# Performance work log

Measured on AMD Instinct MI355X. Metric: run time of the kernel, lower is better.

Reference implementation:

```python
import jax, jax.numpy as jnp
import numpy as np

NUM_HEADS = 16
NEG_INF = float('-inf')


def setup_inputs() -> dict:
    key = jax.random.key(0)
    ks = jax.random.split(key, 8)
    B, S, D = 2, 2048, 1024
    return {
        "query": jax.random.normal(ks[0], (B, S, D), jnp.float32),
        "key": jax.random.normal(ks[1], (B, S, D), jnp.float32),
        "value": jax.random.normal(ks[2], (B, S, D), jnp.float32),
        "attention_mask": jnp.zeros((B, S, S), dtype=bool),
        "Wq": jax.random.normal(ks[3], (D, D), jnp.float32) * (D ** -0.5),
        "Wk": jax.random.normal(ks[4], (D, D), jnp.float32) * (D ** -0.5),
        "Wv": jax.random.normal(ks[5], (D, D), jnp.float32) * (D ** -0.5),
        "Wout": jax.random.normal(ks[6], (D, D), jnp.float32) * (D ** -0.5),
        "b_out": jnp.zeros((D,), jnp.float32),
        "is_causal": 1,
    }


def reference(query, key, value, attention_mask, Wq, Wk, Wv, Wout, b_out, is_causal):
    B, q_len, D = query.shape
    k_len = key.shape[1]
    H = NUM_HEADS
    dk = D // H
    # projections (torch Linear: x @ W.T), split heads -> [B, H, S, dk]
    q = (query @ Wq.T).reshape(B, q_len, H, dk).transpose(0, 2, 1, 3)
    k = (key @ Wk.T).reshape(B, k_len, H, dk).transpose(0, 2, 1, 3)
    v = (value @ Wv.T).reshape(B, k_len, H, dk).transpose(0, 2, 1, 3)
    scores = jnp.einsum('bhqd,bhkd->bhqk', q, k) / jnp.sqrt(jnp.float32(dk))
    if is_causal:
        causal = jnp.triu(jnp.ones((q_len, k_len), dtype=bool), k=1)
        scores = jnp.where(causal, NEG_INF, scores)
    # attn_mask True -> masked out; broadcast over heads
    scores = jnp.where(attention_mask[:, None, :, :], NEG_INF, scores)
    attn = jax.nn.softmax(scores, axis=-1)
    attn = jnp.where(jnp.isnan(attn), 0.0, attn)  # fully-masked rows -> 0
    out = jnp.einsum('bhqk,bhkd->bhqd', attn, v)
    out = out.transpose(0, 2, 1, 3).reshape(B, q_len, D)
    return out @ Wout.T + b_out
```

## Files before the change

### kernel.cpp

```cpp
#include <hip/hip_runtime.h>
#include <hip/hip_bf16.h>

typedef __attribute__((ext_vector_type(8))) short bf16x8;
typedef __attribute__((ext_vector_type(4))) float f32x4;
typedef unsigned long long u64;
typedef unsigned int u32;

#define MFMA(a,b,c) __builtin_amdgcn_mfma_f32_16x16x32_bf16(a,b,c,0,0,0)
#define NEG_INF (-__builtin_inff())
#define SCALE2 0.1803368801111244f

__device__ __forceinline__ unsigned short f2b(float f) {
  unsigned int u = __float_as_uint(f);
  u = u + 0x7fffu + ((u >> 16) & 1u);
  return (unsigned short)(u >> 16);
}

__device__ __forceinline__ u32 pkbf(float lo, float hi) {
  __hip_bfloat162 h = __float22bfloat162_rn(float2{lo, hi});
  return *reinterpret_cast<u32*>(&h);
}

__device__ __forceinline__ void gload_lds16(const unsigned short* g, unsigned short* l) {
  __builtin_amdgcn_global_load_lds((const __attribute__((address_space(1))) void*)g,
                                   (__attribute__((address_space(3))) void*)l, 16, 0, 0);
}

__global__ void cvt7(const float* s0, const float* s1, const float* s2,
                     const float* s3, const float* s4, const float* s5, const float* s6,
                     unsigned short* d0, unsigned short* d1, unsigned short* d2,
                     unsigned short* d3, unsigned short* d4, unsigned short* d5, unsigned short* d6,
                     int nbig, int nsmall) {
  const float* s; unsigned short* d; int n4;
  switch (blockIdx.y) {
    case 0: s=s0; d=d0; n4=nbig; break;
    case 1: s=s1; d=d1; n4=nbig; break;
    case 2: s=s2; d=d2; n4=nbig; break;
    case 3: s=s3; d=d3; n4=nsmall; break;
    case 4: s=s4; d=d4; n4=nsmall; break;
    case 5: s=s5; d=d5; n4=nsmall; break;
    default: s=s6; d=d6; n4=nsmall; break;
  }
  int i = blockIdx.x * blockDim.x + threadIdx.x;
  if (i < n4) {
    float4 v = reinterpret_cast<const float4*>(s)[i];
    ushort4 o;
    o.x = f2b(v.x); o.y = f2b(v.y); o.z = f2b(v.z); o.w = f2b(v.w);
    reinterpret_cast<ushort4*>(d)[i] = o;
  }
}

__global__ void pack_mask(const unsigned char* __restrict__ am, u64* __restrict__ pm, int nU) {
  int lane = threadIdx.x & 63;
  int wid = blockIdx.x * (blockDim.x >> 6) + (threadIdx.x >> 6);
  int stride = gridDim.x * (blockDim.x >> 6);
  for (int u = wid; u < nU; u += stride) {
    unsigned char v = am[(size_t)u * 64 + lane];
    u64 m = __ballot(v != 0);
    if (lane == 0) pm[u] = m;
  }
}

__global__ void mask_summary(const u64* __restrict__ pm, u32* __restrict__ ms, int rows, int nkt) {
  int lane = threadIdx.x & 63;
  int wid = (blockIdx.x * blockDim.x + threadIdx.x) >> 6;
  int nw = (gridDim.x * blockDim.x) >> 6;
  for (int rp = wid; rp < (rows >> 1); rp += nw) {
    int row = rp * 2 + (lane >> 5);
    int t = lane & 31;
    u64 v = pm[(size_t)row * nkt + t];
    u64 bm = __ballot(v != 0ULL);
    if (lane == 0)  ms[rp*2]     = (u32)bm;
    if (lane == 32) ms[rp*2 + 1] = (u32)(bm >> 32);
  }
}

__global__ __launch_bounds__(256) void qkv128s(
    const unsigned short* __restrict__ A,
    const unsigned short* __restrict__ Bw,
    unsigned short* __restrict__ Cqk,
    unsigned short* __restrict__ Cv)
{
  const int K = 1024;
  __shared__ unsigned short As[128*32];
  __shared__ unsigned short Bs[128*32];
  const int tid  = threadIdx.x;
  const int w    = tid >> 6, lane = tid & 63;
  const int wr   = w >> 1,   wc   = w & 1;
  const int g    = lane >> 4, li  = lane & 15;
  const int m0   = blockIdx.x * 128, n0 = blockIdx.y * 128;
  const int bq0  = (m0 >> 12) * 1024 + n0;

  f32x4 acc[4][4] = {};

  const int rS0 = (w*2+0)*16 + (lane>>2);
  const int rS1 = (w*2+1)*16 + (lane>>2);
  const int cS  = (lane&3)*8;
  const unsigned short* gA0 = A  + (size_t)(m0+rS0)*K + cS;
  const unsigned short* gA1 = A  + (size_t)(m0+rS1)*K + cS;
  const unsigned short* gB0 = Bw + (size_t)(bq0+rS0)*K + cS;
  const unsigned short* gB1 = Bw + (size_t)(bq0+rS1)*K + cS;
  unsigned short* lA0 = &As[(w*2+0)*512];
  unsigned short* lA1 = &As[(w*2+1)*512];
  unsigned short* lB0 = &Bs[(w*2+0)*512];
  unsigned short* lB1 = &Bs[(w*2+1)*512];

  for (int k0 = 0; k0 < K; k0 += 32) {
    gload_lds16(gA0 + k0, lA0);
    gload_lds16(gA1 + k0, lA1);
    gload_lds16(gB0 + k0, lB0);
    gload_lds16(gB1 + k0, lB1);
    __syncthreads();

    bf16x8 af[4], bf[4];
    #pragma unroll
    for (int i = 0; i < 4; ++i)
      af[i] = *(const bf16x8*)(&As[(wr*64 + i*16 + li)*32 + g*8]);
    #pragma unroll
    for (int j = 0; j < 4; ++j)
      bf[j] = *(const bf16x8*)(&Bs[(wc*64 + j*16 + li)*32 + g*8]);
    #pragma unroll
    for (int i = 0; i < 4; ++i)
      #pragma unroll
      for (int j = 0; j < 4; ++j)
        acc[i][j] = MFMA(af[i], bf[j], acc[i][j]);
    __syncthreads();
  }

  #pragma unroll
  for (int i = 0; i < 4; ++i) {
    #pragma unroll
    for (int j = 0; j < 4; ++j) {
      int col = n0 + wc*64 + j*16 + li;
      #pragma unroll
      for (int r = 0; r < 4; ++r) {
        int row = m0 + wr*64 + i*16 + g*4 + r;
        float v = acc[i][j][r];
        if (row < 8192) {
          size_t addr = (((size_t)(row >> 11) * 16 + (col >> 6)) * 2048 + (row & 2047)) * 64 + (col & 63);
          Cqk[addr] = f2b(v);
        } else {
          int tk = row & 4095;
          size_t addr = (((size_t)(tk >> 11) * 16 + (col >> 6)) * 64 + (col & 63)) * 2048 + (tk & 2047);
          Cv[addr] = f2b(v);
        }
      }
    }
  }
}

__global__ __launch_bounds__(256) void gemm64db(
    const unsigned short* __restrict__ A,
    const unsigned short* __restrict__ Bw,
    float* __restrict__ Cf,
    const float* __restrict__ bias,
    int M, int N, int K)
{
  const int NT = 32;
  __shared__ unsigned short As[2][64*32];
  __shared__ unsigned short Bs[2][128*32];
  const int tid  = threadIdx.x;
  const int w    = tid >> 6, lane = tid & 63;
  const int wr   = w >> 1,   wc   = w & 1;
  const int g    = lane >> 4, li  = lane & 15;
  const int m0   = blockIdx.x * 64, n0 = blockIdx.y * 128;

  f32x4 acc[2][4] = {};
  const int crow = lane >> 2, ccol = (lane & 3) * 8;
  const unsigned short* gA  = A  + (size_t)(m0 + w*16 + crow)*K + ccol;
  const unsigned short* gB0 = Bw + (size_t)(n0 + w*16 + crow)*K + ccol;
  const unsigned short* gB1 = Bw + (size_t)(n0 + (w+4)*16 + crow)*K + ccol;

  gload_lds16(gA,  &As[0][w*512]);
  gload_lds16(gB0, &Bs[0][w*512]);
  gload_lds16(gB1, &Bs[0][(w+4)*512]);
  __syncthreads();

  for (int t = 0; t < NT; ++t) {
    const int cur = t & 1;
    if (t + 1 < NT) {
      const int k1 = (t + 1) * 32;
      gload_lds16(gA  + k1, &As[cur^1][w*512]);
      gload_lds16(gB0 + k1, &Bs[cur^1][w*512]);
      gload_lds16(gB1 + k1, &Bs[cur^1][(w+4)*512]);
    }
    bf16x8 af[2], bf[4];
    #pragma unroll
    for (int i = 0; i < 2; ++i)
      af[i] = *(const bf16x8*)(&As[cur][(wr*32 + i*16 + li)*32 + g*8]);
    #pragma unroll
    for (int j = 0; j < 4; ++j)
      bf[j] = *(const bf16x8*)(&Bs[cur][(wc*64 + j*16 + li)*32 + g*8]);
    #pragma unroll
    for (int i = 0; i < 2; ++i)
      #pragma unroll
      for (int j = 0; j < 4; ++j)
        acc[i][j] = MFMA(af[i], bf[j], acc[i][j]);
    __syncthreads();
  }

  #pragma unroll
  for (int i = 0; i < 2; ++i) {
    #pragma unroll
    for (int j = 0; j < 4; ++j) {
      int col = n0 + wc*64 + j*16 + li;
      #pragma unroll
      for (int r = 0; r < 4; ++r) {
        int row = m0 + wr*32 + i*16 + g*4 + r;
        Cf[(size_t)row*N + col] = acc[i][j][r] + bias[col];
      }
    }
  }
}

__global__ __launch_bounds__(256, 4) void attn_kernel(
    const unsigned short* __restrict__ Qh,
    const unsigned short* __restrict__ Kh,
    const unsigned short* __restrict__ Vt,
    const u64* __restrict__ pmask,
    const u32* __restrict__ msum,
    const int* __restrict__ causal_p,
    unsigned short* __restrict__ Ob,
    int B, int H, int S)
{
  __shared__ unsigned short Ks [64*64];
  __shared__ unsigned short Vts[64*64];

  const int tid = threadIdx.x, w = tid >> 6, lane = tid & 63;
  const int g = lane >> 4, li = lane & 15;
  const int nkt = S >> 6, nqt = S >> 6;
  const int causal = causal_p[0];

  int id = blockIdx.x;
  int par = (id ^ (id >> 8)) & 1;
  int qh  = ((id >> 1) & 15) ^ (((id >> 8) & 3) << 2);
  int bh  = id >> 5;
  int qt  = par ? (nqt - 1 - qh) : qh;
  const int q0 = qt << 6;
  const int b = bh / H, h = bh % H;
  const size_t baseK = (size_t)bh * S * 64;
  const size_t baseV = (size_t)bh * 64 * S;

  const int qg = q0 + w*16 + li;
  const unsigned short* qp = Qh + baseK + (size_t)qg*64 + g*8;
  const bf16x8 qf0 = *(const bf16x8*)(qp);
  const bf16x8 qf1 = *(const bf16x8*)(qp + 32);

  const u32 sOr = msum[(size_t)b*S + qg];

  f32x4 oacc[4] = {};
  float mrun = -1e30f, lrun = 0.f;

  const int colk  = (lane & 7) ^ ((lane >> 3) & 7);
  const int ldrow = lane >> 3;
  const int ntile = causal ? (qt + 1) : nkt;

  for (int t = 0; t < ntile; ++t) {
    const int kv0 = t << 6;
    __syncthreads();
    #pragma unroll
    for (int s2 = 0; s2 < 2; ++s2) {
      int u = w*2 + s2;
      gload_lds16(Kh + baseK + (size_t)(kv0 + u*8 + ldrow)*64 + colk*8, &Ks[u*512]);
      gload_lds16(Vt + baseV + (size_t)(u*8 + ldrow)*S + kv0 + colk*8, &Vts[u*512]);
    }
    __syncthreads();

    f32x4 sa[4];
    #pragma unroll
    for (int ni = 0; ni < 4; ++ni) sa[ni] = (f32x4){0.f, 0.f, 0.f, 0.f};
    #pragma unroll
    for (int ni = 0; ni < 4; ++ni) {
      int row = ni*16 + li, rx = row & 7;
      bf16x8 k0 = *(const bf16x8*)(&Ks[row*64 + ((g     ^ rx))*8]);
      bf16x8 k1 = *(const bf16x8*)(&Ks[row*64 + (((4+g) ^ rx))*8]);
      sa[ni] = MFMA(k0, qf0, sa[ni]);
      sa[ni] = MFMA(k1, qf1, sa[ni]);
    }

    const bool edge   = (causal != 0) && (t == ntile - 1);
    const bool doMask = __any(((sOr >> t) & 1u) != 0u);
    float corr = 1.0f;
    bool rescale = true;

    if (!edge && !doMask) {
      float pe[4][4];
      #pragma unroll
      for (int ni = 0; ni < 4; ++ni)
        #pragma unroll
        for (int r = 0; r < 4; ++r)
          pe[ni][r] = exp2f(fmaf(sa[ni][r], SCALE2, -mrun));
      float a0 = fmaxf(sa[0][0], sa[0][1]), a1 = fmaxf(sa[0][2], sa[0][3]);
      float a2 = fmaxf(sa[1][0], sa[1][1]), a3 = fmaxf(sa[1][2], sa[1][3]);
      float a4 = fmaxf(sa[2][0], sa[2][1]), a5 = fmaxf(sa[2][2], sa[2][3]);
      float a6 = fmaxf(sa[3][0], sa[3][1]), a7 = fmaxf(sa[3][2], sa[3][3]);
      float mx = fmaxf(fmaxf(fmaxf(a0,a1), fmaxf(a2,a3)),
                       fmaxf(fmaxf(a4,a5), fmaxf(a6,a7)));
      mx = fmaxf(mx, __shfl_xor(mx, 16));
      mx = fmaxf(mx, __shfl_xor(mx, 32));
      float mxs = mx * SCALE2;
      if (__all(mxs <= mrun + 8.0f)) {
        float s0 = (pe[0][0]+pe[0][1]) + (pe[0][2]+pe[0][3]);
        float s1 = (pe[1][0]+pe[1][1]) + (pe[1][2]+pe[1][3]);
        float s2 = (pe[2][0]+pe[2][1]) + (pe[2][2]+pe[2][3]);
        float s3 = (pe[3][0]+pe[3][1]) + (pe[3][2]+pe[3][3]);
        float rs = (s0+s1) + (s2+s3);
        rs += __shfl_xor(rs, 16);
        rs += __shfl_xor(rs, 32);
        lrun += rs;
        #pragma unroll
        for (int ni = 0; ni < 4; ++ni)
          #pragma unroll
          for (int r = 0; r < 4; ++r)
            sa[ni][r] = pe[ni][r];
        rescale = false;
      } else {
        float mu = fmaxf(mrun, mxs);
        corr = exp2f(mrun - mu);
        float rs = 0.f;
        #pragma unroll
        for (int ni = 0; ni < 4; ++ni)
          #pragma unroll
          for (int r = 0; r < 4; ++r) {
            float p = exp2f(fmaf(sa[ni][r], SCALE2, -mu));
            sa[ni][r] = p;
            rs += p;
          }
        rs += __shfl_xor(rs, 16);
        rs += __shfl_xor(rs, 32);
        lrun = lrun * corr + rs;
        mrun = mu;
      }
    } else {
      u64 mrow = doMask ? pmask[((size_t)b*S + qg) * nkt + t] : 0ULL;
      #pragma unroll
      for (int ni = 0; ni < 4; ++ni)
        #pragma unroll
        for (int r = 0; r < 4; ++r) {
          int kvloc = ni*16 + g*4 + r;
          bool dead = (edge && (kv0 + kvloc > qg)) || ((mrow >> kvloc) & 1ULL);
          sa[ni][r] = dead ? NEG_INF : sa[ni][r] * SCALE2;
        }
      float mx = sa[0][0];
      #pragma unroll
      for (int ni = 0; ni < 4; ++ni)
        #pragma unroll
        for (int r = 0; r < 4; ++r)
          if (ni + r) mx = fmaxf(mx, sa[ni][r]);
      mx = fmaxf(mx, __shfl_xor(mx, 16));
      mx = fmaxf(mx, __shfl_xor(mx, 32));
      float mu = fmaxf(mrun, mx);
      corr = exp2f(mrun - mu);
      float rs = 0.f;
      #pragma unroll
      for (int ni = 0; ni < 4; ++ni)
        #pragma unroll
        for (int r = 0; r < 4; ++r) {
          float pe = exp2f(sa[ni][r] - mu);
          sa[ni][r] = pe;
          rs += pe;
        }
      rs += __shfl_xor(rs, 16);
      rs += __shfl_xor(rs, 32);
      lrun = lrun * corr + rs;
      mrun = mu;
    }

    bf16x8 pf[2];
    #pragma unroll
    for (int c = 0; c < 2; ++c) {
      u32 PA0 = pkbf(sa[2*c  ][0], sa[2*c  ][1]);
      u32 PA1 = pkbf(sa[2*c  ][2], sa[2*c  ][3]);
      u32 PB0 = pkbf(sa[2*c+1][0], sa[2*c+1][1]);
      u32 PB1 = pkbf(sa[2*c+1][2], sa[2*c+1][3]);
      u32 X16_0 = (u32)__shfl_xor((int)((g==2) ? PB0 : PA0), 16);
      u32 X16_1 = (u32)__shfl_xor((int)((g==2) ? PB1 : PA1), 16);
      u32 X32_0 = (u32)__shfl_xor((int)((g==0) ? PB0 : PA0), 32);
      u32 X32_1 = (u32)__shfl_xor((int)((g==0) ? PB1 : PA1), 32);
      u32 X48_0 = (u32)__shfl_xor((int)((g==1) ? PB0 : PA0), 48);
      u32 X48_1 = (u32)__shfl_xor((int)((g==1) ? PB1 : PA1), 48);
      union { u32 u[4]; bf16x8 v; } pbu;
      pbu.u[0] = (g==0) ? PA0   : (g==1) ? X48_0 : (g==2) ? X32_0 : X16_0;
      pbu.u[1] = (g==0) ? PA1   : (g==1) ? X48_1 : (g==2) ? X32_1 : X16_1;
      pbu.u[2] = (g==0) ? X16_0 : (g==1) ? X32_0 : (g==2) ? X48_0 : PB0;
      pbu.u[3] = (g==0) ? X16_1 : (g==1) ? X32_1 : (g==2) ? X48_1 : PB1;
      pf[c] = pbu.v;
    }

    if (rescale) {
      #pragma unroll
      for (int di = 0; di < 4; ++di) {
        oacc[di][0] *= corr; oacc[di][1] *= corr;
        oacc[di][2] *= corr; oacc[di][3] *= corr;
      }
    }

    #pragma unroll
    for (int c = 0; c < 2; ++c) {
      #pragma unroll
      for (int di = 0; di < 4; ++di) {
        int d = di*16 + li;
        bf16x8 vf = *(const bf16x8*)(&Vts[d*64 + (((c*4+g) ^ (d&7)))*8]);
        oacc[di] = MFMA(vf, pf[c], oacc[di]);
      }
    }
  }

  __syncthreads();
  unsigned short* scr = &Ks[w*1024];
  float rl = (lrun > 0.f) ? 1.0f / lrun : 0.f;
  #pragma unroll
  for (int di = 0; di < 4; ++di)
    #pragma unroll
    for (int r = 0; r < 4; ++r) {
      int d = di*16 + g*4 + r;
      scr[li*64 + (((d>>3) ^ (li&7)))*8 + (d&7)] = f2b(oacc[di][r] * rl);
    }
  const int D = H * 64;
  #pragma unroll
  for (int rr = 0; rr < 2; ++rr) {
    int q = rr*8 + (lane >> 3);
    int sl = lane & 7;
    bf16x8 v = *(const bf16x8*)(&scr[q*64 + ((sl ^ (q & 7)))*8]);
    *(bf16x8*)(Ob + (size_t)(b*S + q0 + w*16 + q)*D + h*64 + sl*8) = v;
  }
}

extern "C" void kernel_launch(void* const* d_in, const int* in_sizes, int n_in,
                              void* d_out, int out_size, void* d_ws, size_t ws_size,
                              hipStream_t stream) {
  const float* query = (const float*)d_in[0];
  const float* key_  = (const float*)d_in[1];
  const float* value = (const float*)d_in[2];
  const unsigned char* amask = (const unsigned char*)d_in[3];
  const float* Wq   = (const float*)d_in[4];
  const float* Wk   = (const float*)d_in[5];
  const float* Wv   = (const float*)d_in[6];
  const float* Wout = (const float*)d_in[7];
  const float* b_out = (const float*)d_in[8];
  const int* is_causal = (const int*)d_in[9];
  float* out = (float*)d_out;

  const int B = 2, S = 2048, D = 1024, H = 16;
  const int M = B * S;
  const size_t nx = (size_t)M * D;
  const size_t nw = (size_t)D * D;
  const int nU = B * S * (S / 64);

  unsigned short* ws = (unsigned short*)d_ws;
  unsigned short* xq = ws;
  unsigned short* xk = xq + nx;
  unsigned short* xv = xk + nx;
  unsigned short* wq = xv + nx;
  unsigned short* wk = wq + nw;
  unsigned short* wv = wk + nw;
  unsigned short* wo = wv + nw;
  unsigned short* qb = wo + nw;
  unsigned short* kb = qb + nx;
  unsigned short* vt = kb + nx;
  u32* msum = (u32*)(vt + nx);
  unsigned short* ob = xq;
  u64* pmask = (u64*)xv;

  cvt7<<<dim3((unsigned)(nx/4/256), 7), 256, 0, stream>>>(
      query, key_, value, Wq, Wk, Wv, Wout,
      xq, xk, xv, wq, wk, wv, wo, (int)(nx/4), (int)(nw/4));

  qkv128s<<<dim3(3*M/128, D/128), 256, 0, stream>>>(xq, wq, qb, vt);

  pack_mask<<<512, 256, 0, stream>>>(amask, pmask, nU);
  mask_summary<<<128, 256, 0, stream>>>(pmask, msum, M, S/64);

  attn_kernel<<<dim3((S/64) * B * H), 256, 0, stream>>>(qb, kb, vt, pmask, msum, is_causal, ob, B, H, S);

  gemm64db<<<dim3(M/64, D/128), 256, 0, stream>>>(ob, wo, out, b_out, M, D, D);
}
```

Baseline: 168.3 us.

## Pair low and high causal query tiles per block to share K/V loads

Each attention block now handles two query tiles, qt and nqt-1-qt, so causal work is balanced across blocks. The K/V tiles loaded into LDS are reused by both query tiles, which roughly halves global K/V traffic for the low tile. The grid shrinks to 512 blocks, each doing more work with double the accumulator registers. This may lower occupancy and cut parallelism on a large GPU. The bh=id&31 indexing hardcodes B*H=32.

```diff
diff --git a/kernel.cpp b/kernel.cpp
--- a/kernel.cpp
+++ b/kernel.cpp
@@ -213,6 +213,151 @@
   }
 }
 
+__device__ __forceinline__ void attn_tile(
+    const unsigned short* __restrict__ Ks, const unsigned short* __restrict__ Vts,
+    const bf16x8& qf0, const bf16x8& qf1,
+    float& mrun, float& lrun, f32x4* oacc,
+    bool edge, bool doMask, const u64* __restrict__ prow,
+    int t, int kv0, int qg, int g, int li)
+{
+  f32x4 sa[4];
+  #pragma unroll
+  for (int ni = 0; ni < 4; ++ni) sa[ni] = (f32x4){0.f, 0.f, 0.f, 0.f};
+  #pragma unroll
+  for (int ni = 0; ni < 4; ++ni) {
+    int row = ni*16 + li, rx = row & 7;
+    bf16x8 k0 = *(const bf16x8*)(&Ks[row*64 + ((g     ^ rx))*8]);
+    bf16x8 k1 = *(const bf16x8*)(&Ks[row*64 + (((4+g) ^ rx))*8]);
+    sa[ni] = MFMA(k0, qf0, sa[ni]);
+    sa[ni] = MFMA(k1, qf1, sa[ni]);
+  }
+
+  float corr = 1.0f;
+  bool rescale = true;
+
+  if (!edge && !doMask) {
+    float pe[4][4];
+    #pragma unroll
+    for (int ni = 0; ni < 4; ++ni)
+      #pragma unroll
+      for (int r = 0; r < 4; ++r)
+        pe[ni][r] = exp2f(fmaf(sa[ni][r], SCALE2, -mrun));
+    float a0 = fmaxf(sa[0][0], sa[0][1]), a1 = fmaxf(sa[0][2], sa[0][3]);
+    float a2 = fmaxf(sa[1][0], sa[1][1]), a3 = fmaxf(sa[1][2], sa[1][3]);
+    float a4 = fmaxf(sa[2][0], sa[2][1]), a5 = fmaxf(sa[2][2], sa[2][3]);
+    float a6 = fmaxf(sa[3][0], sa[3][1]), a7 = fmaxf(sa[3][2], sa[3][3]);
+    float mx = fmaxf(fmaxf(fmaxf(a0,a1), fmaxf(a2,a3)),
+                     fmaxf(fmaxf(a4,a5), fmaxf(a6,a7)));
+    mx = fmaxf(mx, __shfl_xor(mx, 16));
+    mx = fmaxf(mx, __shfl_xor(mx, 32));
+    float mxs = mx * SCALE2;
+    if (__all(mxs <= mrun + 8.0f)) {
+      float s0 = (pe[0][0]+pe[0][1]) + (pe[0][2]+pe[0][3]);
+      float s1 = (pe[1][0]+pe[1][1]) + (pe[1][2]+pe[1][3]);
+      float s2 = (pe[2][0]+pe[2][1]) + (pe[2][2]+pe[2][3]);
+      float s3 = (pe[3][0]+pe[3][1]) + (pe[3][2]+pe[3][3]);
+      float rs = (s0+s1) + (s2+s3);
+      rs += __shfl_xor(rs, 16);
+      rs += __shfl_xor(rs, 32);
+      lrun += rs;
+      #pragma unroll
+      for (int ni = 0; ni < 4; ++ni)
+        #pragma unroll
+        for (int r = 0; r < 4; ++r)
+          sa[ni][r] = pe[ni][r];
+      rescale = false;
+    } else {
+      float mu = fmaxf(mrun, mxs);
+      corr = exp2f(mrun - mu);
+      float rs = 0.f;
+      #pragma unroll
+      for (int ni = 0; ni < 4; ++ni)
+        #pragma unroll
+        for (int r = 0; r < 4; ++r) {
+          float p = exp2f(fmaf(sa[ni][r], SCALE2, -mu));
+          sa[ni][r] = p;
+          rs += p;
+        }
+      rs += __shfl_xor(rs, 16);
+      rs += __shfl_xor(rs, 32);
+      lrun = lrun * corr + rs;
+      mrun = mu;
+    }
+  } else {
+    u64 mrow = doMask ? prow[t] : 0ULL;
+    #pragma unroll
+    for (int ni = 0; ni < 4; ++ni)
+      #pragma unroll
+      for (int r = 0; r < 4; ++r) {
+        int kvloc = ni*16 + g*4 + r;
+        bool dead = (edge && (kv0 + kvloc > qg)) || ((mrow >> kvloc) & 1ULL);
+        sa[ni][r] = dead ? NEG_INF : sa[ni][r] * SCALE2;
+      }
+    float mx = sa[0][0];
+    #pragma unroll
+    for (int ni = 0; ni < 4; ++ni)
+      #pragma unroll
+      for (int r = 0; r < 4; ++r)
+        if (ni + r) mx = fmaxf(mx, sa[ni][r]);
+    mx = fmaxf(mx, __shfl_xor(mx, 16));
+    mx = fmaxf(mx, __shfl_xor(mx, 32));
+    float mu = fmaxf(mrun, mx);
+    corr = exp2f(mrun - mu);
+    float rs = 0.f;
+    #pragma unroll
+    for (int ni = 0; ni < 4; ++ni)
+      #pragma unroll
+      for (int r = 0; r < 4; ++r) {
+        float pe = exp2f(sa[ni][r] - mu);
+        sa[ni][r] = pe;
+        rs += pe;
+      }
+    rs += __shfl_xor(rs, 16);
+    rs += __shfl_xor(rs, 32);
+    lrun = lrun * corr + rs;
+    mrun = mu;
+  }
+
+  bf16x8 pf[2];
+  #pragma unroll
+  for (int c = 0; c < 2; ++c) {
+    u32 PA0 = pkbf(sa[2*c  ][0], sa[2*c  ][1]);
+    u32 PA1 = pkbf(sa[2*c  ][2], sa[2*c  ][3]);
+    u32 PB0 = pkbf(sa[2*c+1][0], sa[2*c+1][1]);
+    u32 PB1 = pkbf(sa[2*c+1][2], sa[2*c+1][3]);
+    u32 X16_0 = (u32)__shfl_xor((int)((g==2) ? PB0 : PA0), 16);
+    u32 X16_1 = (u32)__shfl_xor((int)((g==2) ? PB1 : PA1), 16);
+    u32 X32_0 = (u32)__shfl_xor((int)((g==0) ? PB0 : PA0), 32);
+    u32 X32_1 = (u32)__shfl_xor((int)((g==0) ? PB1 : PA1), 32);
+    u32 X48_0 = (u32)__shfl_xor((int)((g==1) ? PB0 : PA0), 48);
+    u32 X48_1 = (u32)__shfl_xor((int)((g==1) ? PB1 : PA1), 48);
+    union { u32 u[4]; bf16x8 v; } pbu;
+    pbu.u[0] = (g==0) ? PA0   : (g==1) ? X48_0 : (g==2) ? X32_0 : X16_0;
+    pbu.u[1] = (g==0) ? PA1   : (g==1) ? X48_1 : (g==2) ? X32_1 : X16_1;
+    pbu.u[2] = (g==0) ? X16_0 : (g==1) ? X32_0 : (g==2) ? X48_0 : PB0;
+    pbu.u[3] = (g==0) ? X16_1 : (g==1) ? X32_1 : (g==2) ? X48_1 : PB1;
+    pf[c] = pbu.v;
+  }
+
+  if (rescale) {
+    #pragma unroll
+    for (int di = 0; di < 4; ++di) {
+      oacc[di][0] *= corr; oacc[di][1] *= corr;
+      oacc[di][2] *= corr; oacc[di][3] *= corr;
+    }
+  }
+
+  #pragma unroll
+  for (int c = 0; c < 2; ++c) {
+    #pragma unroll
+    for (int di = 0; di < 4; ++di) {
+      int d = di*16 + li;
+      bf16x8 vf = *(const bf16x8*)(&Vts[d*64 + (((c*4+g) ^ (d&7)))*8]);
+      oacc[di] = MFMA(vf, pf[c], oacc[di]);
+    }
+  }
+}
+
 __global__ __launch_bounds__(256, 4) void attn_kernel(
     const unsigned short* __restrict__ Qh,
     const unsigned short* __restrict__ Kh,
@@ -228,34 +373,42 @@
 
   const int tid = threadIdx.x, w = tid >> 6, lane = tid & 63;
   const int g = lane >> 4, li = lane & 15;
-  const int nkt = S >> 6, nqt = S >> 6;
+  const int nkt = S >> 6;
   const int causal = causal_p[0];
 
-  int id = blockIdx.x;
-  int par = (id ^ (id >> 8)) & 1;
-  int qh  = ((id >> 1) & 15) ^ (((id >> 8) & 3) << 2);
-  int bh  = id >> 5;
-  int qt  = par ? (nqt - 1 - qh) : qh;
-  const int q0 = qt << 6;
-  const int b = bh / H, h = bh % H;
+  const int id = blockIdx.x;
+  const int bh = id & 31;
+  const int qp = id >> 5;
+  const int qtL = qp, qtH = nkt - 1 - qp;
+  const int q0L = qtL << 6, q0H = qtH << 6;
+  const int b = bh >> 4, h = bh & 15;
   const size_t baseK = (size_t)bh * S * 64;
   const size_t baseV = (size_t)bh * 64 * S;
 
-  const int qg = q0 + w*16 + li;
-  const unsigned short* qp = Qh + baseK + (size_t)qg*64 + g*8;
-  const bf16x8 qf0 = *(const bf16x8*)(qp);
-  const bf16x8 qf1 = *(const bf16x8*)(qp + 32);
-
-  const u32 sOr = msum[(size_t)b*S + qg];
-
-  f32x4 oacc[4] = {};
-  float mrun = -1e30f, lrun = 0.f;
+  const int qgL = q0L + w*16 + li;
+  const int qgH = q0H + w*16 + li;
+  const unsigned short* qpL = Qh + baseK + (size_t)qgL*64 + g*8;
+  const unsigned short* qpH = Qh + baseK + (size_t)qgH*64 + g*8;
+  const bf16x8 qfL0 = *(const bf16x8*)(qpL);
+  const bf16x8 qfL1 = *(const bf16x8*)(qpL + 32);
+  const bf16x8 qfH0 = *(const bf16x8*)(qpH);
+  const bf16x8 qfH1 = *(const bf16x8*)(qpH + 32);
+
+  const u32 sOrL = msum[(size_t)b*S + qgL];
+  const u32 sOrH = msum[(size_t)b*S + qgH];
+  const u64* prowL = pmask + (size_t)(b*S + qgL) * nkt;
+  const u64* prowH = pmask + (size_t)(b*S + qgH) * nkt;
+
+  f32x4 oaccL[4] = {}, oaccH[4] = {};
+  float mrunL = -1e30f, lrunL = 0.f;
+  float mrunH = -1e30f, lrunH = 0.f;
 
   const int colk  = (lane & 7) ^ ((lane >> 3) & 7);
   const int ldrow = lane >> 3;
-  const int ntile = causal ? (qt + 1) : nkt;
-
-  for (int t = 0; t < ntile; ++t) {
+  const int ntL = causal ? (qtL + 1) : nkt;
+  const int ntH = causal ? (qtH + 1) : nkt;
+
+  for (int t = 0; t < ntH; ++t) {
     const int kv0 = t << 6;
     __syncthreads();
     #pragma unroll
@@ -266,163 +419,43 @@
     }
     __syncthreads();
 
-    f32x4 sa[4];
-    #pragma unroll
-    for (int ni = 0; ni < 4; ++ni) sa[ni] = (f32x4){0.f, 0.f, 0.f, 0.f};
-    #pragma unroll
-    for (int ni = 0; ni < 4; ++ni) {
-      int row = ni*16 + li, rx = row & 7;
-      bf16x8 k0 = *(const bf16x8*)(&Ks[row*64 + ((g     ^ rx))*8]);
-      bf16x8 k1 = *(const bf16x8*)(&Ks[row*64 + (((4+g) ^ rx))*8]);
-      sa[ni] = MFMA(k0, qf0, sa[ni]);
-      sa[ni] = MFMA(k1, qf1, sa[ni]);
-    }
-
-    const bool edge   = (causal != 0) && (t == ntile - 1);
-    const bool doMask = __any(((sOr >> t) & 1u) != 0u);
-    float corr = 1.0f;
-    bool rescale = true;
-
-    if (!edge && !doMask) {
-      float pe[4][4];
-      #pragma unroll
-      for (int ni = 0; ni < 4; ++ni)
-        #pragma unroll
-        for (int r = 0; r < 4; ++r)
-          pe[ni][r] = exp2f(fmaf(sa[ni][r], SCALE2, -mrun));
-      float a0 = fmaxf(sa[0][0], sa[0][1]), a1 = fmaxf(sa[0][2], sa[0][3]);
-      float a2 = fmaxf(sa[1][0], sa[1][1]), a3 = fmaxf(sa[1][2], sa[1][3]);
-      float a4 = fmaxf(sa[2][0], sa[2][1]), a5 = fmaxf(sa[2][2], sa[2][3]);
-      float a6 = fmaxf(sa[3][0], sa[3][1]), a7 = fmaxf(sa[3][2], sa[3][3]);
-      float mx = fmaxf(fmaxf(fmaxf(a0,a1), fmaxf(a2,a3)),
-                       fmaxf(fmaxf(a4,a5), fmaxf(a6,a7)));
-      mx = fmaxf(mx, __shfl_xor(mx, 16));
-      mx = fmaxf(mx, __shfl_xor(mx, 32));
-      float mxs = mx * SCALE2;
-      if (__all(mxs <= mrun + 8.0f)) {
-        float s0 = (pe[0][0]+pe[0][1]) + (pe[0][2]+pe[0][3]);
-        float s1 = (pe[1][0]+pe[1][1]) + (pe[1][2]+pe[1][3]);
-        float s2 = (pe[2][0]+pe[2][1]) + (pe[2][2]+pe[2][3]);
-        float s3 = (pe[3][0]+pe[3][1]) + (pe[3][2]+pe[3][3]);
-        float rs = (s0+s1) + (s2+s3);
-        rs += __shfl_xor(rs, 16);
-        rs += __shfl_xor(rs, 32);
-        lrun += rs;
-        #pragma unroll
-        for (int ni = 0; ni < 4; ++ni)
-          #pragma unroll
-          for (int r = 0; r < 4; ++r)
-            sa[ni][r] = pe[ni][r];
-        rescale = false;
-      } else {
-        float mu = fmaxf(mrun, mxs);
-        corr = exp2f(mrun - mu);
-        float rs = 0.f;
-        #pragma unroll
-        for (int ni = 0; ni < 4; ++ni)
-          #pragma unroll
-          for (int r = 0; r < 4; ++r) {
-            float p = exp2f(fmaf(sa[ni][r], SCALE2, -mu));
-            sa[ni][r] = p;
-            rs += p;
-          }
-        rs += __shfl_xor(rs, 16);
-        rs += __shfl_xor(rs, 32);
-        lrun = lrun * corr + rs;
-        mrun = mu;
-      }
-    } else {
-      u64 mrow = doMask ? pmask[((size_t)b*S + qg) * nkt + t] : 0ULL;
-      #pragma unroll
-      for (int ni = 0; ni < 4; ++ni)
-        #pragma unroll
-        for (int r = 0; r < 4; ++r) {
-          int kvloc = ni*16 + g*4 + r;
-          bool dead = (edge && (kv0 + kvloc > qg)) || ((mrow >> kvloc) & 1ULL);
-          sa[ni][r] = dead ? NEG_INF : sa[ni][r] * SCALE2;
-        }
-      float mx = sa[0][0];
-      #pragma unroll
-      for (int ni = 0; ni < 4; ++ni)
-        #pragma unroll
-        for (int r = 0; r < 4; ++r)
-          if (ni + r) mx = fmaxf(mx, sa[ni][r]);
-      mx = fmaxf(mx, __shfl_xor(mx, 16));
-      mx = fmaxf(mx, __shfl_xor(mx, 32));
-      float mu = fmaxf(mrun, mx);
-      corr = exp2f(mrun - mu);
-      float rs = 0.f;
-      #pragma unroll
-      for (int ni = 0; ni < 4; ++ni)
-        #pragma unroll
-        for (int r = 0; r < 4; ++r) {
-          float pe = exp2f(sa[ni][r] - mu);
-          sa[ni][r] = pe;
-          rs += pe;
-        }
-      rs += __shfl_xor(rs, 16);
-      rs += __shfl_xor(rs, 32);
-      lrun = lrun * corr + rs;
-      mrun = mu;
-    }
-
-    bf16x8 pf[2];
-    #pragma unroll
-    for (int c = 0; c < 2; ++c) {
-      u32 PA0 = pkbf(sa[2*c  ][0], sa[2*c  ][1]);
-      u32 PA1 = pkbf(sa[2*c  ][2], sa[2*c  ][3]);
-      u32 PB0 = pkbf(sa[2*c+1][0], sa[2*c+1][1]);
-      u32 PB1 = pkbf(sa[2*c+1][2], sa[2*c+1][3]);
-      u32 X16_0 = (u32)__shfl_xor((int)((g==2) ? PB0 : PA0), 16);
-      u32 X16_1 = (u32)__shfl_xor((int)((g==2) ? PB1 : PA1), 16);
-      u32 X32_0 = (u32)__shfl_xor((int)((g==0) ? PB0 : PA0), 32);
-      u32 X32_1 = (u32)__shfl_xor((int)((g==0) ? PB1 : PA1), 32);
-      u32 X48_0 = (u32)__shfl_xor((int)((g==1) ? PB0 : PA0), 48);
-      u32 X48_1 = (u32)__shfl_xor((int)((g==1) ? PB1 : PA1), 48);
-      union { u32 u[4]; bf16x8 v; } pbu;
-      pbu.u[0] = (g==0) ? PA0   : (g==1) ? X48_0 : (g==2) ? X32_0 : X16_0;
-      pbu.u[1] = (g==0) ? PA1   : (g==1) ? X48_1 : (g==2) ? X32_1 : X16_1;
-      pbu.u[2] = (g==0) ? X16_0 : (g==1) ? X32_0 : (g==2) ? X48_0 : PB0;
-      pbu.u[3] = (g==0) ? X16_1 : (g==1) ? X32_1 : (g==2) ? X48_1 : PB1;
-      pf[c] = pbu.v;
-    }
-
-    if (rescale) {
-      #pragma unroll
-      for (int di = 0; di < 4; ++di) {
-        oacc[di][0] *= corr; oacc[di][1] *= corr;
-        oacc[di][2] *= corr; oacc[di][3] *= corr;
-      }
-    }
-
-    #pragma unroll
-    for (int c = 0; c < 2; ++c) {
-      #pragma unroll
-      for (int di = 0; di < 4; ++di) {
-        int d = di*16 + li;
-        bf16x8 vf = *(const bf16x8*)(&Vts[d*64 + (((c*4+g) ^ (d&7)))*8]);
-        oacc[di] = MFMA(vf, pf[c], oacc[di]);
-      }
+    {
+      const bool edge   = (causal != 0) && (t == ntH - 1);
+      const bool doMask = __any(((sOrH >> t) & 1u) != 0u);
+      attn_tile(Ks, Vts, qfH0, qfH1, mrunH, lrunH, oaccH,
+                edge, doMask, prowH, t, kv0, qgH, g, li);
+    }
+    if (t < ntL) {
+      const bool edge   = (causal != 0) && (t == ntL - 1);
+      const bool doMask = __any(((sOrL >> t) & 1u) != 0u);
+      attn_tile(Ks, Vts, qfL0, qfL1, mrunL, lrunL, oaccL,
+                edge, doMask, prowL, t, kv0, qgL, g, li);
     }
   }
 
   __syncthreads();
-  unsigned short* scr = &Ks[w*1024];
-  float rl = (lrun > 0.f) ? 1.0f / lrun : 0.f;
+  const int D = H * 64;
+  unsigned short* scrL = &Ks[w*1024];
+  unsigned short* scrH = &Vts[w*1024];
+  float rlL = (lrunL > 0.f) ? 1.0f / lrunL : 0.f;
+  float rlH = (lrunH > 0.f) ? 1.0f / lrunH : 0.f;
   #pragma unroll
   for (int di = 0; di < 4; ++di)
     #pragma unroll
     for (int r = 0; r < 4; ++r) {
       int d = di*16 + g*4 + r;
-      scr[li*64 + (((d>>3) ^ (li&7)))*8 + (d&7)] = f2b(oacc[di][r] * rl);
-    }
-  const int D = H * 64;
+      int slot = ((d>>3) ^ (li&7));
+      scrL[li*64 + slot*8 + (d&7)] = f2b(oaccL[di][r] * rlL);
+      scrH[li*64 + slot*8 + (d&7)] = f2b(oaccH[di][r] * rlH);
+    }
   #pragma unroll
   for (int rr = 0; rr < 2; ++rr) {
     int q = rr*8 + (lane >> 3);
     int sl = lane & 7;
-    bf16x8 v = *(const bf16x8*)(&scr[q*64 + ((sl ^ (q & 7)))*8]);
-    *(bf16x8*)(Ob + (size_t)(b*S + q0 + w*16 + q)*D + h*64 + sl*8) = v;
+    bf16x8 vL = *(const bf16x8*)(&scrL[q*64 + ((sl ^ (q & 7)))*8]);
+    bf16x8 vH = *(const bf16x8*)(&scrH[q*64 + ((sl ^ (q & 7)))*8]);
+    *(bf16x8*)(Ob + (size_t)(b*S + q0L + w*16 + q)*D + h*64 + sl*8) = vL;
+    *(bf16x8*)(Ob + (size_t)(b*S + q0H + w*16 + q)*D + h*64 + sl*8) = vH;
   }
 }
 
@@ -471,7 +504,7 @@
   pack_mask<<<512, 256, 0, stream>>>(amask, pmask, nU);
   mask_summary<<<128, 256, 0, stream>>>(pmask, msum, M, S/64);
 
-  attn_kernel<<<dim3((S/64) * B * H), 256, 0, stream>>>(qb, kb, vt, pmask, msum, is_causal, ob, B, H, S);
+  attn_kernel<<<dim3((S/128) * B * H), 256, 0, stream>>>(qb, kb, vt, pmask, msum, is_causal, ob, B, H, S);
 
   gemm64db<<<dim3(M/64, D/128), 256, 0, stream>>>(ob, wo, out, b_out, M, D, D);
 }
```

New measurement: 214.9 us. +27.7%, slower.
